# Kernel optimization log

Hardware: AMD Instinct MI355X
Metric: run time of the kernel (lower is better)

The kernel has to match this reference:

```python
import math
import jax, jax.numpy as jnp
import numpy as np

ANCHOR_AREAS = [4 * 4, 16 * 16, 64 * 64, 128 * 128]
ASPECT_RATIOS = [1 / 2.0, 1 / 1.0, 2 / 1.0]
SCALE_RATIOS = [1.0, 2.0, 3 / 4.0]
NUM_ANCHORS = len(ASPECT_RATIOS) * len(SCALE_RATIOS)  # 9


def _anchor_wh():
    wh = []
    for s in ANCHOR_AREAS:
        for ar in ASPECT_RATIOS:
            h = math.sqrt(s / ar)
            w = ar * h
            for sr in SCALE_RATIOS:
                wh.append([w * sr, h * sr])
    return np.asarray(wh, np.float32).reshape(len(ANCHOR_AREAS), NUM_ANCHORS, 2)


def build_anchor_boxes(input_size):
    """All anchors in (cx, cy, w, h), shape [A, 4]. Static numpy computation."""
    wh = _anchor_wh()
    out = []
    for i in range(len(ANCHOR_AREAS)):
        fm = int(math.ceil(input_size / 2.0 ** (i + 2)))
        grid = input_size / fm
        centers = (np.arange(fm, dtype=np.float32) + 0.5) * grid
        gx, gy = np.meshgrid(centers, centers)  # gx varies along width
        xy = np.stack([gx, gy], axis=-1)  # [fm, fm, 2]
        xy = np.broadcast_to(xy[:, :, None, :], (fm, fm, NUM_ANCHORS, 2))
        whl = np.broadcast_to(wh[i][None, None, :, :], (fm, fm, NUM_ANCHORS, 2))
        out.append(np.concatenate([xy, whl], axis=-1).reshape(-1, 4))
    return jnp.asarray(np.concatenate(out, 0), jnp.float32)


def box_iou_xywh(anchors, boxes):
    """anchors [A,4] xywh, boxes [B,N,4] xywh -> IoU [B,A,N] (kuangliu +1 convention)."""
    a1 = jnp.concatenate([anchors[:, :2] - anchors[:, 2:] / 2,
                          anchors[:, :2] + anchors[:, 2:] / 2], axis=-1)  # [A,4]
    b1 = jnp.concatenate([boxes[..., :2] - boxes[..., 2:] / 2,
                          boxes[..., :2] + boxes[..., 2:] / 2], axis=-1)  # [B,N,4]
    lt = jnp.maximum(a1[None, :, None, :2], b1[:, None, :, :2])  # [B,A,N,2]
    rb = jnp.minimum(a1[None, :, None, 2:], b1[:, None, :, 2:])
    wh = jnp.clip(rb - lt + 1.0, 0.0)
    inter = wh[..., 0] * wh[..., 1]  # [B,A,N]
    area_a = (a1[:, 2] - a1[:, 0] + 1.0) * (a1[:, 3] - a1[:, 1] + 1.0)  # [A]
    area_b = (b1[..., 2] - b1[..., 0] + 1.0) * (b1[..., 3] - b1[..., 1] + 1.0)  # [B,N]
    return inter / (area_a[None, :, None] + area_b[:, None, :] - inter)


def setup_inputs() -> dict:
    key = jax.random.key(0)
    k1, k2, k3 = jax.random.split(key, 3)
    B, N, S = 4, 64, 512
    # valid xyxy boxes inside the image
    x1y1 = jax.random.uniform(k1, (B, N, 2), jnp.float32, 0.0, S - 130.0)
    wh = jax.random.uniform(k2, (B, N, 2), jnp.float32, 4.0, 128.0)
    boxes = jnp.concatenate([x1y1, x1y1 + wh], axis=-1)
    labels = jax.random.randint(k3, (B, N), 0, 10, jnp.int64 if jax.config.jax_enable_x64 else jnp.int32)
    return {"labels": labels, "boxes": boxes, "input_size": S}


def reference(labels, boxes, input_size):
    B = boxes.shape[0]
    anchors = build_anchor_boxes(int(input_size))  # [A,4] xywh
    # xyxy -> xywh (kuangliu: center (a+b)/2, size b-a+1)
    a, b = boxes[..., :2], boxes[..., 2:]
    boxes_xywh = jnp.concatenate([(a + b) / 2.0, b - a + 1.0], axis=-1)  # [B,N,4]
    ious = box_iou_xywh(anchors, boxes_xywh)  # [B,A,N]
    max_ious = jnp.max(ious, axis=2)  # [B,A]
    max_ids = jnp.argmax(ious, axis=2)  # [B,A]
    gather = jax.vmap(lambda t, i: t[i])
    matched = gather(boxes_xywh, max_ids)  # [B,A,4]
    loc_xy = (matched[..., :2] - anchors[None, :, :2]) / anchors[None, :, 2:]
    loc_wh = jnp.log(matched[..., 2:] / anchors[None, :, 2:])
    loc_targets = jnp.concatenate([loc_xy, loc_wh], axis=-1)  # [B,A,4]
    cls = gather(labels, max_ids)  # [B,A]
    cls = jnp.where(max_ious < 0.5, 0, cls)
    cls = jnp.where((max_ious > 0.4) & (max_ious < 0.5), -1, cls)
    return cls, loc_targets
```

## Files before the change

kernel.cpp:

```cpp
#include <hip/hip_runtime.h>
#include <math.h>


__global__ __launch_bounds__(256) void anchors_kernel(
    const int*   __restrict__ labels,
    const float* __restrict__ boxes,
    float*       __restrict__ out,
    int B, int N, int A, int S)
{
    __shared__ float4 s_corn[64];
    __shared__ float  s_area[64];
    __shared__ float4 s_xywh[64];
    __shared__ int    s_lab[64];
    __shared__ float4 s_box0;
    __shared__ int    s_lab0;
    __shared__ int    s_Lb;

    const int gid = blockIdx.x * 256 + threadIdx.x;
    const int b = gid / A;
    const int t = threadIdx.x;

    const int a0 = blockIdx.x * 256 - b * A;
    int r0 = a0;
    int lvl = 0;
    int fm  = S >> 2;
    #pragma unroll
    for (int i = 0; i < 3; ++i) {
        int cnt = fm * fm * 9;
        if (r0 >= cnt) { r0 -= cnt; lvl = i + 1; fm >>= 1; }
    }
    const int lfm = 31 - __clz(fm);
    const float grid = (float)(4 << lvl);
    const float sl   = (float)((lvl == 3) ? 128 : (4 << (2 * lvl)));

    const int cell_lo = r0 / 9;
    const int cell_hi = (r0 + 255) / 9;
    const int ci_lo = cell_lo >> lfm, ci_hi = cell_hi >> lfm;
    int cj_lo, cj_hi;
    if (ci_lo == ci_hi) { cj_lo = cell_lo & (fm - 1); cj_hi = cell_hi & (fm - 1); }
    else                { cj_lo = 0;                  cj_hi = fm - 1; }
    const float ext = 1.41422f * sl + 0.5f;
    const float bbx1 = ((float)cj_lo + 0.5f) * grid - ext;
    const float bbx2 = ((float)cj_hi + 0.5f) * grid + ext;
    const float bby1 = ((float)ci_lo + 0.5f) * grid - ext;
    const float bby2 = ((float)ci_hi + 0.5f) * grid + ext;

    if (t < 64) {
        bool pred = false;
        float cx = 0, cy = 0, w = 0, h = 0, bx1 = 0, by1 = 0, bx2 = 0, by2 = 0;
        int lab = 0;
        if (t < N && b < B) {
            float4 bx = reinterpret_cast<const float4*>(boxes)[b * N + t];
            cx = (bx.x + bx.z) * 0.5f;
            cy = (bx.y + bx.w) * 0.5f;
            w  = bx.z - bx.x + 1.0f;
            h  = bx.w - bx.y + 1.0f;
            bx1 = cx - w * 0.5f;
            by1 = cy - h * 0.5f;
            bx2 = cx + w * 0.5f;
            by2 = cy + h * 0.5f;
            lab = labels[b * N + t];
            pred = (fminf(bbx2, bx2) - fmaxf(bbx1, bx1) + 1.0f > 0.0f) &&
                   (fminf(bby2, by2) - fmaxf(bby1, by1) + 1.0f > 0.0f);
        }
        unsigned long long mask = __ballot(pred);
        if (pred) {
            int pos = __popcll(mask & ((1ull << t) - 1ull));
            s_corn[pos] = make_float4(bx1, by1, bx2, by2);
            s_area[pos] = (bx2 - bx1 + 1.0f) * (by2 - by1 + 1.0f);
            s_xywh[pos] = make_float4(cx, cy, w, h);
            s_lab[pos]  = lab;
        }
        if (t == 0) {
            s_Lb   = __popcll(mask);
            s_box0 = make_float4(cx, cy, w, h);
            s_lab0 = lab;
        }
    }
    __syncthreads();

    const int r    = r0 + t;
    const int k    = r % 9;
    const int cell = r / 9;
    const int cj   = cell & (fm - 1);
    const int ci   = cell >> lfm;

    const int ar_i = (k >= 6) ? 2 : ((k >= 3) ? 1 : 0);
    const int sr_i = k - 3 * ar_i;
    const double s2  = sqrt(2.0);
    const double hb  = (ar_i == 0) ? s2 : (ar_i == 1 ? 1.0 : 0.5 * s2);
    const double wb  = (ar_i == 0) ? 0.5 * s2 : (ar_i == 1 ? 1.0 : s2);
    const double srd = (sr_i == 0) ? 1.0 : (sr_i == 1 ? 2.0 : 0.75);
    const float  aw  = (float)(wb * srd) * sl;
    const float  ah  = (float)(hb * srd) * sl;

    const float acx = ((float)cj + 0.5f) * grid;
    const float acy = ((float)ci + 0.5f) * grid;
    const float ax1 = acx - aw * 0.5f;
    const float ay1 = acy - ah * 0.5f;
    const float ax2 = acx + aw * 0.5f;
    const float ay2 = acy + ah * 0.5f;
    const float area_a = (ax2 - ax1 + 1.0f) * (ay2 - ay1 + 1.0f);

    float best_in = 0.0f, best_un = 1.0f;
    int   bj = -1;
    const int L = s_Lb;
    for (int j = 0; j < L; ++j) {
        float4 c = s_corn[j];
        float iw = fmaxf(fminf(ax2, c.z) - fmaxf(ax1, c.x) + 1.0f, 0.0f);
        float ih = fmaxf(fminf(ay2, c.w) - fmaxf(ay1, c.y) + 1.0f, 0.0f);
        float in_ = iw * ih;
        float un_ = (area_a + s_area[j]) - in_;
        bool better = (in_ * best_un) > (best_in * un_);
        best_in = better ? in_ : best_in;
        best_un = better ? un_ : best_un;
        bj      = better ? j   : bj;
    }

    if (gid >= B * A) return;

    float best, mcx, mcy, mw, mh;
    int lab;
    if (bj >= 0) {
        best = best_in / best_un;
        float4 m = s_xywh[bj];
        mcx = m.x; mcy = m.y; mw = m.z; mh = m.w;
        lab = s_lab[bj];
    } else {
        best = 0.0f;
        float4 m = s_box0;
        mcx = m.x; mcy = m.y; mw = m.z; mh = m.w;
        lab = s_lab0;
    }

    int cls = lab;
    if (best < 0.5f) cls = 0;
    if (best > 0.4f && best < 0.5f) cls = -1;
    out[(size_t)gid] = (float)cls;

    float4 loc;
    loc.x = (mcx - acx) / aw;
    loc.y = (mcy - acy) / ah;
    loc.z = __logf(mw / aw);
    loc.w = __logf(mh / ah);
    reinterpret_cast<float4*>(out + (size_t)B * A)[gid] = loc;
}

extern "C" void kernel_launch(void* const* d_in, const int* in_sizes, int n_in,
                              void* d_out, int out_size, void* d_ws, size_t ws_size,
                              hipStream_t stream) {
    const int S = 512;
    int A = 0;
    for (int i = 0; i < 4; ++i) {
        int f = (S + (1 << (i + 2)) - 1) >> (i + 2);
        A += f * f * 9;
    }
    const int B = out_size / (5 * A);
    const int N = in_sizes[0] / B;

    const int total  = B * A;
    const int blocks = (total + 255) / 256;

    anchors_kernel<<<blocks, 256, 0, stream>>>(
        (const int*)d_in[0], (const float*)d_in[1], (float*)d_out, B, N, A, S);
}
```

Baseline: 18.23 us.

## Cull boxes per wavefront instead of per block and drop the barrier

Each 64-lane wavefront now loads all boxes, culls them against its own tighter anchor bounding region, and compacts survivors into its own shared-memory slice. This removes the block-wide __syncthreads, since each wavefront only reads what it wrote itself. The tighter per-wave region should also shrink the IoU loop trip count. Divisions are replaced with hardware reciprocal multiplies, which may slightly change rounding. Intra-wave shared-memory visibility without a barrier relies on lockstep wavefront execution.

```diff
diff --git a/kernel.cpp b/kernel.cpp
--- a/kernel.cpp
+++ b/kernel.cpp
@@ -8,76 +8,71 @@
     float*       __restrict__ out,
     int B, int N, int A, int S)
 {
-    __shared__ float4 s_corn[64];
-    __shared__ float  s_area[64];
-    __shared__ float4 s_xywh[64];
-    __shared__ int    s_lab[64];
-    __shared__ float4 s_box0;
-    __shared__ int    s_lab0;
-    __shared__ int    s_Lb;
+    __shared__ float4 s_corn[256];
+    __shared__ float  s_area[256];
+    __shared__ float4 s_xywh[256];
+    __shared__ int    s_lab[256];
+    __shared__ float4 s_b0[4];
+    __shared__ int    s_l0[4];
 
-    const int gid = blockIdx.x * 256 + threadIdx.x;
-    const int b = gid / A;
-    const int t = threadIdx.x;
+    const int t    = threadIdx.x;
+    const int lane = t & 63;
+    const int wid  = t >> 6;
+    const int gid  = blockIdx.x * 256 + t;
 
-    const int a0 = blockIdx.x * 256 - b * A;
-    int r0 = a0;
-    int lvl = 0;
-    int fm  = S >> 2;
+    const int b  = (blockIdx.x * 256) / A;
+    int r0 = blockIdx.x * 256 - b * A;
+    int lvl = 0, fm = S >> 2;
     #pragma unroll
     for (int i = 0; i < 3; ++i) {
         int cnt = fm * fm * 9;
         if (r0 >= cnt) { r0 -= cnt; lvl = i + 1; fm >>= 1; }
     }
-    const int lfm = 31 - __clz(fm);
+    const int   lfm  = 31 - __clz(fm);
     const float grid = (float)(4 << lvl);
     const float sl   = (float)((lvl == 3) ? 128 : (4 << (2 * lvl)));
 
-    const int cell_lo = r0 / 9;
-    const int cell_hi = (r0 + 255) / 9;
+    const int wr0     = r0 + wid * 64;
+    const int cell_lo = wr0 / 9;
+    const int cell_hi = (wr0 + 63) / 9;
     const int ci_lo = cell_lo >> lfm, ci_hi = cell_hi >> lfm;
     int cj_lo, cj_hi;
     if (ci_lo == ci_hi) { cj_lo = cell_lo & (fm - 1); cj_hi = cell_hi & (fm - 1); }
     else                { cj_lo = 0;                  cj_hi = fm - 1; }
-    const float ext = 1.41422f * sl + 0.5f;
+    const float ext  = 1.41422f * sl + 0.5f;
     const float bbx1 = ((float)cj_lo + 0.5f) * grid - ext;
     const float bbx2 = ((float)cj_hi + 0.5f) * grid + ext;
     const float bby1 = ((float)ci_lo + 0.5f) * grid - ext;
     const float bby2 = ((float)ci_hi + 0.5f) * grid + ext;
 
-    if (t < 64) {
-        bool pred = false;
+    int L;
+    {
+        bool  pred = false;
         float cx = 0, cy = 0, w = 0, h = 0, bx1 = 0, by1 = 0, bx2 = 0, by2 = 0;
-        int lab = 0;
-        if (t < N && b < B) {
-            float4 bx = reinterpret_cast<const float4*>(boxes)[b * N + t];
+        int   lab = 0;
+        if (lane < N) {
+            float4 bx = reinterpret_cast<const float4*>(boxes)[b * N + lane];
             cx = (bx.x + bx.z) * 0.5f;
             cy = (bx.y + bx.w) * 0.5f;
             w  = bx.z - bx.x + 1.0f;
             h  = bx.w - bx.y + 1.0f;
-            bx1 = cx - w * 0.5f;
-            by1 = cy - h * 0.5f;
-            bx2 = cx + w * 0.5f;
-            by2 = cy + h * 0.5f;
-            lab = labels[b * N + t];
+            bx1 = cx - w * 0.5f;  by1 = cy - h * 0.5f;
+            bx2 = cx + w * 0.5f;  by2 = cy + h * 0.5f;
+            lab = labels[b * N + lane];
             pred = (fminf(bbx2, bx2) - fmaxf(bbx1, bx1) + 1.0f > 0.0f) &&
                    (fminf(bby2, by2) - fmaxf(bby1, by1) + 1.0f > 0.0f);
         }
         unsigned long long mask = __ballot(pred);
         if (pred) {
-            int pos = __popcll(mask & ((1ull << t) - 1ull));
+            int pos = wid * 64 + __popcll(mask & ((1ull << lane) - 1ull));
             s_corn[pos] = make_float4(bx1, by1, bx2, by2);
             s_area[pos] = (bx2 - bx1 + 1.0f) * (by2 - by1 + 1.0f);
             s_xywh[pos] = make_float4(cx, cy, w, h);
             s_lab[pos]  = lab;
         }
-        if (t == 0) {
-            s_Lb   = __popcll(mask);
-            s_box0 = make_float4(cx, cy, w, h);
-            s_lab0 = lab;
-        }
+        if (lane == 0) { s_b0[wid] = make_float4(cx, cy, w, h); s_l0[wid] = lab; }
+        L = __popcll(mask);
     }
-    __syncthreads();
 
     const int r    = r0 + t;
     const int k    = r % 9;
@@ -104,46 +99,49 @@
 
     float best_in = 0.0f, best_un = 1.0f;
     int   bj = -1;
-    const int L = s_Lb;
+    const int base = wid * 64;
     for (int j = 0; j < L; ++j) {
-        float4 c = s_corn[j];
+        float4 c = s_corn[base + j];
         float iw = fmaxf(fminf(ax2, c.z) - fmaxf(ax1, c.x) + 1.0f, 0.0f);
         float ih = fmaxf(fminf(ay2, c.w) - fmaxf(ay1, c.y) + 1.0f, 0.0f);
         float in_ = iw * ih;
-        float un_ = (area_a + s_area[j]) - in_;
+        float un_ = (area_a + s_area[base + j]) - in_;
         bool better = (in_ * best_un) > (best_in * un_);
         best_in = better ? in_ : best_in;
         best_un = better ? un_ : best_un;
         bj      = better ? j   : bj;
     }
 
-    if (gid >= B * A) return;
-
     float best, mcx, mcy, mw, mh;
     int lab;
     if (bj >= 0) {
         best = best_in / best_un;
-        float4 m = s_xywh[bj];
+        float4 m = s_xywh[base + bj];
         mcx = m.x; mcy = m.y; mw = m.z; mh = m.w;
-        lab = s_lab[bj];
+        lab = s_lab[base + bj];
     } else {
         best = 0.0f;
-        float4 m = s_box0;
+        float4 m = s_b0[wid];
         mcx = m.x; mcy = m.y; mw = m.z; mh = m.w;
-        lab = s_lab0;
+        lab = s_l0[wid];
     }
 
     int cls = lab;
     if (best < 0.5f) cls = 0;
     if (best > 0.4f && best < 0.5f) cls = -1;
-    out[(size_t)gid] = (float)cls;
 
+    const float rcp_aw = __builtin_amdgcn_rcpf(aw);
+    const float rcp_ah = __builtin_amdgcn_rcpf(ah);
     float4 loc;
-    loc.x = (mcx - acx) / aw;
-    loc.y = (mcy - acy) / ah;
-    loc.z = __logf(mw / aw);
-    loc.w = __logf(mh / ah);
-    reinterpret_cast<float4*>(out + (size_t)B * A)[gid] = loc;
+    loc.x = (mcx - acx) * rcp_aw;
+    loc.y = (mcy - acy) * rcp_ah;
+    loc.z = __logf(mw * rcp_aw);
+    loc.w = __logf(mh * rcp_ah);
+
+    if (gid < B * A) {
+        out[(size_t)gid] = (float)cls;
+        reinterpret_cast<float4*>(out + (size_t)B * A)[gid] = loc;
+    }
 }
 
 extern "C" void kernel_launch(void* const* d_in, const int* in_sizes, int n_in,
```

New measurement: 17.34 us. -4.9%, faster.
